# Performance work log

Measured on AMD Instinct MI355X. Metric: run time of the kernel, lower is better.

Reference implementation:

```python
import jax, jax.numpy as jnp
import numpy as np

HID = 768
POS = 768
TGT = 20
LBL = 30522
EPS = 1e-5


def layer_norm(x, g, b):
    mu = jnp.mean(x, axis=-1, keepdims=True)
    var = jnp.mean((x - mu) ** 2, axis=-1, keepdims=True)
    return (x - mu) * jax.lax.rsqrt(var + EPS) * g + b


def setup_inputs() -> dict:
    key = jax.random.key(0)
    ks = jax.random.split(key, 12)
    bs, n_node, num_pairs = 4, 512, 128
    inp = {
        "input_nodes": jax.random.normal(ks[0], (bs, n_node, HID), dtype=jnp.float32),
        "pairs": jax.random.randint(ks[1], (bs, num_pairs, 2), 0, n_node - 1, dtype=jnp.int64),
        "pos_emb": jax.random.normal(ks[2], (TGT, POS), dtype=jnp.float32) * 0.02,
        "W1": jax.random.normal(ks[3], (2 * HID + POS, HID), dtype=jnp.float32) * 0.02,
        "b1": jnp.zeros((HID,), dtype=jnp.float32),
        "g1": jnp.ones((HID,), dtype=jnp.float32),
        "be1": jnp.zeros((HID,), dtype=jnp.float32),
        "W2": jax.random.normal(ks[4], (HID, HID), dtype=jnp.float32) * 0.02,
        "b2": jnp.zeros((HID,), dtype=jnp.float32),
        "g2": jnp.ones((HID,), dtype=jnp.float32),
        "be2": jnp.zeros((HID,), dtype=jnp.float32),
        "Wd": jax.random.normal(ks[5], (HID, LBL), dtype=jnp.float32) * 0.02,
        "bd": jnp.zeros((LBL,), dtype=jnp.float32),
    }
    return inp


def reference(input_nodes, pairs, pos_emb, W1, b1, g1, be1, W2, b2, g2, be2, Wd, bd):
    bs, num_pairs, _ = pairs.shape
    dim = input_nodes.shape[-1]
    left = pairs[:, :, 0] + 1   # [bs, np]
    right = pairs[:, :, 1] + 1
    # gather paired node features: [bs, np, dim]
    lh = jnp.take_along_axis(input_nodes, left[:, :, None], axis=1)
    rh = jnp.take_along_axis(input_nodes, right[:, :, None], axis=1)
    R = bs * num_pairs
    lh = jnp.broadcast_to(lh.reshape(R, 1, dim), (R, TGT, dim))
    rh = jnp.broadcast_to(rh.reshape(R, 1, dim), (R, TGT, dim))
    pe = jnp.broadcast_to(pos_emb[None, :, :], (R, TGT, POS))
    x = jnp.concatenate((lh, rh, pe), axis=-1)  # [R, TGT, 2*HID+POS]
    h = layer_norm(jax.nn.gelu(x @ W1 + b1), g1, be1)
    h = layer_norm(jax.nn.gelu(h @ W2 + b2), g2, be2)
    return h @ Wd + bd  # [R, TGT, LBL]
```

## Files before the change

kernel.cpp:

```cpp
#include <hip/hip_runtime.h>
#include <stdint.h>
#include <math.h>

typedef unsigned short u16;
typedef unsigned int u32;

#define HID   768
#define TGT   20
#define LBL   30522
#define RPAIR 512
#define ROWS  10240
#define KCAT  1536
#define NPAD2 30720

typedef float  f32x4  __attribute__((ext_vector_type(4)));
typedef __bf16 bf16x8 __attribute__((ext_vector_type(8)));

__device__ __forceinline__ u16 f2bf(float f) {
  u32 u = __float_as_uint(f);
  u += 0x7fffu + ((u >> 16) & 1u);
  return (u16)(u >> 16);
}
__device__ __forceinline__ float bf2f(u16 h) {
  return __uint_as_float(((u32)h) << 16);
}
__device__ __forceinline__ float gelu_tanh(float x) {
  float x3 = x * x * x;
  float t = tanhf(0.7978845608028654f * (x + 0.044715f * x3));
  return 0.5f * x * (1.0f + t);
}

__device__ __forceinline__ void async16(u16* lds, const u16* g) {
  __builtin_amdgcn_global_load_lds(
      (__attribute__((address_space(1))) void*)const_cast<u16*>(g),
      (__attribute__((address_space(3))) void*)lds,
      16, 0, 0);
}

#define BARRIER() do { asm volatile("" ::: "memory"); __builtin_amdgcn_s_barrier(); asm volatile("" ::: "memory"); } while (0)
#define VMWAIT8() do { asm volatile("s_waitcnt vmcnt(8)" ::: "memory"); __builtin_amdgcn_sched_barrier(0); } while (0)
#define VMWAIT0() do { asm volatile("s_waitcnt vmcnt(0)" ::: "memory"); __builtin_amdgcn_sched_barrier(0); } while (0)

__global__ __launch_bounds__(256) void tconv_kernel(const float* __restrict__ B,
                                                    u16* __restrict__ Bt,
                                                    int K, int N, int Npad) {
  __shared__ u16 tile[32][34];
  int n0 = blockIdx.x * 32, k0 = blockIdx.y * 32;
  int tx = threadIdx.x & 31, ty = threadIdx.x >> 5;
#pragma unroll
  for (int i = 0; i < 4; i++) {
    int kk = ty + i * 8;
    int k = k0 + kk, n = n0 + tx;
    float v = (k < K && n < N) ? B[(size_t)k * N + n] : 0.0f;
    tile[kk][tx] = f2bf(v);
  }
  __syncthreads();
#pragma unroll
  for (int i = 0; i < 4; i++) {
    int nn = ty + i * 8;
    int n = n0 + nn, k = k0 + tx;
    if (n < Npad && k < K) Bt[(size_t)n * K + k] = tile[tx][nn];
  }
}

__global__ __launch_bounds__(256) void gather_kernel(const float* __restrict__ nodes,
                                                     const int* __restrict__ p32,
                                                     u16* __restrict__ A1) {
  int idx = blockIdx.x * 256 + threadIdx.x;
  if (idx >= RPAIR * KCAT) return;
  bool is64 = ((p32[1] | p32[3] | p32[5] | p32[7] | p32[9] | p32[11] | p32[13] | p32[15]) == 0);
  int r = idx / KCAT, c = idx - r * KCAT;
  int b = r >> 7, p = r & 127;
  int which = (c >= HID) ? 1 : 0;
  int cc = which ? (c - HID) : c;
  int slot = (b * 128 + p) * 2 + which;
  int node = (is64 ? p32[slot * 2] : p32[slot]) + 1;
  float v = nodes[((size_t)(b * 512 + node)) * HID + cc];
  A1[idx] = f2bf(v);
}

__global__ __launch_bounds__(256) void peproj_kernel(const float* __restrict__ pos_emb,
                                                     const float* __restrict__ W1,
                                                     const float* __restrict__ b1,
                                                     float* __restrict__ pep) {
  __shared__ float pe[HID];
  int t = blockIdx.x, tid = threadIdx.x;
  for (int i = tid; i < HID; i += 256) pe[i] = pos_emb[t * HID + i];
  __syncthreads();
  float acc0 = 0.f, acc1 = 0.f, acc2 = 0.f;
  const float* Wp = W1 + (size_t)KCAT * HID;
  for (int k = 0; k < HID; k++) {
    float p = pe[k];
    const float* wr = Wp + (size_t)k * HID;
    acc0 = fmaf(p, wr[tid], acc0);
    acc1 = fmaf(p, wr[tid + 256], acc1);
    acc2 = fmaf(p, wr[tid + 512], acc2);
  }
  pep[t * HID + tid]       = acc0 + b1[tid];
  pep[t * HID + tid + 256] = acc1 + b1[tid + 256];
  pep[t * HID + tid + 512] = acc2 + b1[tid + 512];
}

template <int EPI>
__global__ __launch_bounds__(256) void gemm_bt(const u16* __restrict__ A,
                                               const u16* __restrict__ Bt,
                                               const float* __restrict__ bias,
                                               float* __restrict__ Cf,
                                               u16* __restrict__ Cb,
                                               int N, int K) {
  __shared__ __align__(16) u16 As[128 * 32];
  __shared__ __align__(16) u16 Bs[128 * 32];
  const int tid  = threadIdx.x;
  const int lane = tid & 63;
  const int w    = tid >> 6;
  const int wr   = w >> 1, wc = w & 1;
  const int m0 = blockIdx.y * 128;
  const int n0 = blockIdx.x * 128;

  f32x4 acc[4][4];
  const f32x4 fzero = {0.f, 0.f, 0.f, 0.f};
#pragma unroll
  for (int m = 0; m < 4; m++)
#pragma unroll
    for (int n = 0; n < 4; n++) acc[m][n] = fzero;

  const int srow = lane >> 2;
  const int scol = (lane & 3) * 8;
  const int nkt = K >> 5;

  for (int kt = 0; kt < nkt; ++kt) {
    const int k0 = kt << 5;
#pragma unroll
    for (int j = 0; j < 2; j++) {
      int rbase = w * 32 + j * 16;
      async16(&As[rbase * 32], A + (size_t)(m0 + rbase + srow) * K + k0 + scol);
      async16(&Bs[rbase * 32], Bt + (size_t)(n0 + rbase + srow) * K + k0 + scol);
    }
    asm volatile("s_waitcnt vmcnt(0)" ::: "memory");
    __syncthreads();

    bf16x8 a[4], b[4];
    const int kk = (lane >> 4) * 8;
#pragma unroll
    for (int m = 0; m < 4; m++)
      a[m] = *reinterpret_cast<const bf16x8*>(&As[(wr * 64 + m * 16 + (lane & 15)) * 32 + kk]);
#pragma unroll
    for (int n = 0; n < 4; n++)
      b[n] = *reinterpret_cast<const bf16x8*>(&Bs[(wc * 64 + n * 16 + (lane & 15)) * 32 + kk]);
#pragma unroll
    for (int m = 0; m < 4; m++)
#pragma unroll
      for (int n = 0; n < 4; n++)
        acc[m][n] = __builtin_amdgcn_mfma_f32_16x16x32_bf16(a[m], b[n], acc[m][n], 0, 0, 0);
    __syncthreads();
  }

  const int rr = (lane >> 4) * 4;
  const int cc = lane & 15;
#pragma unroll
  for (int m = 0; m < 4; m++) {
#pragma unroll
    for (int n = 0; n < 4; n++) {
      int col = n0 + wc * 64 + n * 16 + cc;
#pragma unroll
      for (int j = 0; j < 4; j++) {
        int row = m0 + wr * 64 + m * 16 + rr + j;
        float v = acc[m][n][j];
        if (EPI == 0) {
          Cf[(size_t)row * N + col] = v;
        } else {
          v = gelu_tanh(v + bias[col]);
          Cb[(size_t)row * N + col] = f2bf(v);
        }
      }
    }
  }
}

__global__ __launch_bounds__(512, 2) void gemm256_stream(const u16* __restrict__ A,
                                                         const u16* __restrict__ B,
                                                         const float* __restrict__ bias,
                                                         float* __restrict__ C) {
  __shared__ __align__(16) u16 As[2][256 * 64];
  __shared__ __align__(16) u16 Bs[2][256 * 64];
  const int tid  = threadIdx.x;
  const int lane = tid & 63;
  const int wid  = tid >> 6;
  const int wm   = wid >> 2;
  const int wn   = wid & 3;

  const int x  = blockIdx.x & 7;
  const int jb = blockIdx.x >> 3;
  const int t0 = (600 * jb) >> 5;
  const int t1 = (600 * (jb + 1)) >> 5;
  const int Q  = (t1 - t0) * 12;

  f32x4 acc[8][4];
  const f32x4 fzero = {0.f, 0.f, 0.f, 0.f};
#pragma unroll
  for (int mi = 0; mi < 8; mi++)
#pragma unroll
    for (int ni = 0; ni < 4; ni++) acc[mi][ni] = fzero;

  const int sl_r = lane >> 3;
  const int sl_c = ((lane & 7) ^ sl_r) * 8;

  auto stage = [&](int q) {
    int tt = t0 + q / 12;
    int kt = q - (q / 12) * 12;
    int mt = 5 * x + tt / 120;
    int nt = tt - (tt / 120) * 120;
    const int k0 = kt * 64;
    u16* Ab = As[q & 1];
    u16* Bb = Bs[q & 1];
    const u16* Ag = A + (size_t)(mt * 256) * 768 + k0;
    const u16* Bg = B + (size_t)(nt * 256) * 768 + k0;
#pragma unroll
    for (int jj = 0; jj < 4; jj++) {
      int rbase = wid * 32 + jj * 8;
      async16(Ab + rbase * 64, Ag + (size_t)(rbase + sl_r) * 768 + sl_c);
      async16(Bb + rbase * 64, Bg + (size_t)(rbase + sl_r) * 768 + sl_c);
    }
  };
  auto lda = [&](const u16* buf, int mi, int ks) -> bf16x8 {
    int row = wm * 128 + mi * 16 + (lane & 15);
    int kch = ks * 4 + (lane >> 4);
    return *reinterpret_cast<const bf16x8*>(&buf[row * 64 + ((kch ^ (row & 7)) << 3)]);
  };
  auto ldb = [&](const u16* buf, int ni, int ks) -> bf16x8 {
    int row = wn * 64 + ni * 16 + (lane & 15);
    int kch = ks * 4 + (lane >> 4);
    return *reinterpret_cast<const bf16x8*>(&buf[row * 64 + ((kch ^ (row & 7)) << 3)]);
  };

  const int rr  = (lane >> 4) * 4;
  const int ccl = lane & 15;

  stage(0);
  for (int q = 0; q < Q; ++q) {
    if (q + 1 < Q) { stage(q + 1); VMWAIT8(); }
    else          { VMWAIT0(); }
    BARRIER();

    const u16* Ab = As[q & 1];
    const u16* Bb = Bs[q & 1];
#pragma unroll
    for (int ks = 0; ks < 2; ++ks) {
      bf16x8 aF[8], bF[4];
#pragma unroll
      for (int mi = 0; mi < 8; ++mi) aF[mi] = lda(Ab, mi, ks);
#pragma unroll
      for (int ni = 0; ni < 4; ++ni) bF[ni] = ldb(Bb, ni, ks);
      __builtin_amdgcn_s_setprio(1);
#pragma unroll
      for (int mi = 0; mi < 8; ++mi)
#pragma unroll
        for (int ni = 0; ni < 4; ++ni)
          acc[mi][ni] = __builtin_amdgcn_mfma_f32_16x16x32_bf16(aF[mi], bF[ni], acc[mi][ni], 0, 0, 0);
      __builtin_amdgcn_s_setprio(0);
    }

    int kt = q - (q / 12) * 12;
    if (kt == 11) {
      int tt = t0 + q / 12;
      int mt = 5 * x + tt / 120;
      int nt = tt - (tt / 120) * 120;
      int r0 = mt * 256 + wm * 128;
      int c0 = nt * 256 + wn * 64;
#pragma unroll
      for (int ni = 0; ni < 4; ++ni) {
        int col = c0 + ni * 16 + ccl;
        if (col < LBL) {
          float bv = bias[col];
#pragma unroll
          for (int mi = 0; mi < 8; ++mi)
#pragma unroll
            for (int j = 0; j < 4; ++j)
              C[(size_t)(r0 + mi * 16 + rr + j) * LBL + col] = acc[mi][ni][j] + bv;
        }
      }
#pragma unroll
      for (int mi = 0; mi < 8; mi++)
#pragma unroll
        for (int ni = 0; ni < 4; ni++) acc[mi][ni] = fzero;
    }
    BARRIER();
  }
}

__global__ __launch_bounds__(256) void fuse1_kernel(const float* __restrict__ s,
                                                    const float* __restrict__ pep,
                                                    const float* __restrict__ g1,
                                                    const float* __restrict__ be1,
                                                    u16* __restrict__ h1) {
  __shared__ float red[8];
  int g = blockIdx.x, tid = threadIdx.x;
  int r = g / TGT, t = g - r * TGT;
  const float* sr = s + (size_t)r * HID;
  const float* pt = pep + (size_t)t * HID;
  float y[3], s1 = 0.f, s2 = 0.f;
#pragma unroll
  for (int i = 0; i < 3; i++) {
    int j = tid + i * 256;
    float x = sr[j] + pt[j];
    y[i] = gelu_tanh(x);
    s1 += y[i];
    s2 += y[i] * y[i];
  }
#pragma unroll
  for (int off = 32; off > 0; off >>= 1) {
    s1 += __shfl_down(s1, off);
    s2 += __shfl_down(s2, off);
  }
  if ((tid & 63) == 0) { red[tid >> 6] = s1; red[4 + (tid >> 6)] = s2; }
  __syncthreads();
  float mean = (red[0] + red[1] + red[2] + red[3]) * (1.0f / HID);
  float var  = (red[4] + red[5] + red[6] + red[7]) * (1.0f / HID) - mean * mean;
  float inv  = rsqrtf(var + 1e-5f);
#pragma unroll
  for (int i = 0; i < 3; i++) {
    int j = tid + i * 256;
    h1[(size_t)g * HID + j] = f2bf((y[i] - mean) * inv * g1[j] + be1[j]);
  }
}

__global__ __launch_bounds__(256) void fuse2_kernel(const u16* __restrict__ G,
                                                    const float* __restrict__ g2,
                                                    const float* __restrict__ be2,
                                                    u16* __restrict__ h2) {
  __shared__ float red[8];
  int g = blockIdx.x, tid = threadIdx.x;
  const u16* gr = G + (size_t)g * HID;
  float y[3], s1 = 0.f, s2 = 0.f;
#pragma unroll
  for (int i = 0; i < 3; i++) {
    int j = tid + i * 256;
    y[i] = bf2f(gr[j]);
    s1 += y[i];
    s2 += y[i] * y[i];
  }
#pragma unroll
  for (int off = 32; off > 0; off >>= 1) {
    s1 += __shfl_down(s1, off);
    s2 += __shfl_down(s2, off);
  }
  if ((tid & 63) == 0) { red[tid >> 6] = s1; red[4 + (tid >> 6)] = s2; }
  __syncthreads();
  float mean = (red[0] + red[1] + red[2] + red[3]) * (1.0f / HID);
  float var  = (red[4] + red[5] + red[6] + red[7]) * (1.0f / HID) - mean * mean;
  float inv  = rsqrtf(var + 1e-5f);
#pragma unroll
  for (int i = 0; i < 3; i++) {
    int j = tid + i * 256;
    h2[(size_t)g * HID + j] = f2bf((y[i] - mean) * inv * g2[j] + be2[j]);
  }
}

extern "C" void kernel_launch(void* const* d_in, const int* in_sizes, int n_in,
                              void* d_out, int out_size, void* d_ws, size_t ws_size,
                              hipStream_t stream) {
  const float* input_nodes = (const float*)d_in[0];
  const int*   pairs       = (const int*)d_in[1];
  const float* pos_emb     = (const float*)d_in[2];
  const float* W1  = (const float*)d_in[3];
  const float* b1  = (const float*)d_in[4];
  const float* g1  = (const float*)d_in[5];
  const float* be1 = (const float*)d_in[6];
  const float* W2  = (const float*)d_in[7];
  const float* b2  = (const float*)d_in[8];
  const float* g2  = (const float*)d_in[9];
  const float* be2 = (const float*)d_in[10];
  const float* Wd  = (const float*)d_in[11];
  const float* bd  = (const float*)d_in[12];
  float* out = (float*)d_out;

  char* ws = (char*)d_ws;
  u16*   WdT   = (u16*)(ws + 0);
  u16*   W2T   = (u16*)(ws + 47185920);
  u16*   W1lrT = (u16*)(ws + 48365568);
  u16*   A1    = (u16*)(ws + 50724864);
  float* pep   = (float*)(ws + 52297728);
  float* sbuf  = (float*)(ws + 52359168);
  u16*   h1    = (u16*)(ws + 53932032);
  u16*   G     = (u16*)(ws + 69660672);

  tconv_kernel<<<dim3(960, 24), 256, 0, stream>>>(Wd, WdT, HID, LBL, NPAD2);
  tconv_kernel<<<dim3(24, 24), 256, 0, stream>>>(W2, W2T, HID, HID, HID);
  tconv_kernel<<<dim3(24, 48), 256, 0, stream>>>(W1, W1lrT, KCAT, HID, HID);
  gather_kernel<<<dim3((RPAIR * KCAT + 255) / 256), 256, 0, stream>>>(input_nodes, pairs, A1);
  peproj_kernel<<<dim3(TGT), 256, 0, stream>>>(pos_emb, W1, b1, pep);

  gemm_bt<0><<<dim3(6, 4), 256, 0, stream>>>(A1, W1lrT, nullptr, sbuf, nullptr, HID, KCAT);
  fuse1_kernel<<<dim3(ROWS), 256, 0, stream>>>(sbuf, pep, g1, be1, h1);

  gemm_bt<1><<<dim3(6, 80), 256, 0, stream>>>(h1, W2T, b2, nullptr, G, HID, HID);
  fuse2_kernel<<<dim3(ROWS), 256, 0, stream>>>(G, g2, be2, G);

  gemm256_stream<<<dim3(256), 512, 0, stream>>>(G, WdT, bd, out);
}
```

Baseline: 1.181 ms.

## Stage final GEMM epilogue through LDS and overlap its stores with next tile

Restructures the vocabulary GEMM so each output tile's accumulators pass through an LDS buffer and are written as coalesced float4 rows instead of scattered scalar stores. Half the epilogue is issued after the last K step and the rest is deferred into the next tile's first K step, with tuned vmcnt waits so the stores overlap the loads and MFMA work. Tile assignment becomes strided round-robin, and the bias is loaded once per tile as a vector. The extra 32 KB LDS buffer and launch_bounds(512,1) lower the occupancy target, and the hand-counted waitcnt values are fragile.

```diff
diff --git a/kernel.cpp b/kernel.cpp
--- a/kernel.cpp
+++ b/kernel.cpp
@@ -38,8 +38,8 @@
 }
 
 #define BARRIER() do { asm volatile("" ::: "memory"); __builtin_amdgcn_s_barrier(); asm volatile("" ::: "memory"); } while (0)
-#define VMWAIT8() do { asm volatile("s_waitcnt vmcnt(8)" ::: "memory"); __builtin_amdgcn_sched_barrier(0); } while (0)
-#define VMWAIT0() do { asm volatile("s_waitcnt vmcnt(0)" ::: "memory"); __builtin_amdgcn_sched_barrier(0); } while (0)
+#define LBAR() do { asm volatile("s_waitcnt lgkmcnt(0)" ::: "memory"); __builtin_amdgcn_sched_barrier(0); __builtin_amdgcn_s_barrier(); asm volatile("" ::: "memory"); } while (0)
+#define VMW(N) do { asm volatile("s_waitcnt vmcnt(" #N ")" ::: "memory"); __builtin_amdgcn_sched_barrier(0); } while (0)
 
 __global__ __launch_bounds__(256) void tconv_kernel(const float* __restrict__ B,
                                                     u16* __restrict__ Bt,
@@ -177,12 +177,13 @@
   }
 }
 
-__global__ __launch_bounds__(512, 2) void gemm256_stream(const u16* __restrict__ A,
-                                                         const u16* __restrict__ B,
-                                                         const float* __restrict__ bias,
-                                                         float* __restrict__ C) {
+__global__ __launch_bounds__(512, 1) void gemm256_drip(const u16* __restrict__ A,
+                                                       const u16* __restrict__ B,
+                                                       const float* __restrict__ bias,
+                                                       float* __restrict__ C) {
   __shared__ __align__(16) u16 As[2][256 * 64];
   __shared__ __align__(16) u16 Bs[2][256 * 64];
+  __shared__ __align__(16) float ep[32 * 256];
   const int tid  = threadIdx.x;
   const int lane = tid & 63;
   const int wid  = tid >> 6;
@@ -191,28 +192,24 @@
 
   const int x  = blockIdx.x & 7;
   const int jb = blockIdx.x >> 3;
-  const int t0 = (600 * jb) >> 5;
-  const int t1 = (600 * (jb + 1)) >> 5;
-  const int Q  = (t1 - t0) * 12;
+  const int S  = (600 - jb + 31) >> 5;
 
   f32x4 acc[8][4];
   const f32x4 fzero = {0.f, 0.f, 0.f, 0.f};
-#pragma unroll
-  for (int mi = 0; mi < 8; mi++)
-#pragma unroll
-    for (int ni = 0; ni < 4; ni++) acc[mi][ni] = fzero;
 
   const int sl_r = lane >> 3;
   const int sl_c = ((lane & 7) ^ sl_r) * 8;
 
-  auto stage = [&](int q) {
-    int tt = t0 + q / 12;
-    int kt = q - (q / 12) * 12;
-    int mt = 5 * x + tt / 120;
-    int nt = tt - (tt / 120) * 120;
+  auto tileCoord = [&](int s, int& mt, int& nt) {
+    int u = jb + (s << 5);
+    int q5 = u / 5;
+    mt = 5 * x + (u - q5 * 5);
+    nt = q5;
+  };
+
+  auto stageK = [&](int buf, int mt, int nt, int kt) {
     const int k0 = kt * 64;
-    u16* Ab = As[q & 1];
-    u16* Bb = Bs[q & 1];
+    u16* Ab = As[buf]; u16* Bb = Bs[buf];
     const u16* Ag = A + (size_t)(mt * 256) * 768 + k0;
     const u16* Bg = B + (size_t)(nt * 256) * 768 + k0;
 #pragma unroll
@@ -235,57 +232,104 @@
 
   const int rr  = (lane >> 4) * 4;
   const int ccl = lane & 15;
-
-  stage(0);
-  for (int q = 0; q < Q; ++q) {
-    if (q + 1 < Q) { stage(q + 1); VMWAIT8(); }
-    else          { VMWAIT0(); }
-    BARRIER();
-
-    const u16* Ab = As[q & 1];
-    const u16* Bb = Bs[q & 1];
-#pragma unroll
-    for (int ks = 0; ks < 2; ++ks) {
-      bf16x8 aF[8], bF[4];
-#pragma unroll
-      for (int mi = 0; mi < 8; ++mi) aF[mi] = lda(Ab, mi, ks);
-#pragma unroll
-      for (int ni = 0; ni < 4; ++ni) bF[ni] = ldb(Bb, ni, ks);
-      __builtin_amdgcn_s_setprio(1);
-#pragma unroll
-      for (int mi = 0; mi < 8; ++mi)
-#pragma unroll
-        for (int ni = 0; ni < 4; ++ni)
-          acc[mi][ni] = __builtin_amdgcn_mfma_f32_16x16x32_bf16(aF[mi], bF[ni], acc[mi][ni], 0, 0, 0);
-      __builtin_amdgcn_s_setprio(0);
-    }
-
-    int kt = q - (q / 12) * 12;
-    if (kt == 11) {
-      int tt = t0 + q / 12;
-      int mt = 5 * x + tt / 120;
-      int nt = tt - (tt / 120) * 120;
-      int r0 = mt * 256 + wm * 128;
-      int c0 = nt * 256 + wn * 64;
-#pragma unroll
-      for (int ni = 0; ni < 4; ++ni) {
-        int col = c0 + ni * 16 + ccl;
-        if (col < LBL) {
-          float bv = bias[col];
-#pragma unroll
-          for (int mi = 0; mi < 8; ++mi)
-#pragma unroll
-            for (int j = 0; j < 4; ++j)
-              C[(size_t)(r0 + mi * 16 + rr + j) * LBL + col] = acc[mi][ni][j] + bv;
+  const int c4  = (tid & 63) * 4;
+
+  f32x4 b4 = fzero;
+  auto bounce4 = [&](int miBase, int r0t, int c0t, int ntB) {
+#pragma unroll
+    for (int mi0 = 0; mi0 < 4; ++mi0) {
+      int mi = miBase + mi0;
+#pragma unroll
+      for (int ni = 0; ni < 4; ++ni)
+#pragma unroll
+        for (int j = 0; j < 4; ++j)
+          ep[(wm * 16 + rr + j) * 256 + wn * 64 + ni * 16 + ccl] = acc[mi][ni][j];
+      LBAR();
+#pragma unroll
+      for (int p = 0; p < 4; ++p) {
+        int lr = p * 8 + wid;
+        int rowg = r0t + (lr >> 4) * 128 + mi * 16 + (lr & 15);
+        f32x4 v = *reinterpret_cast<const f32x4*>(&ep[lr * 256 + c4]);
+        v += b4;
+        if (ntB != 119) {
+          *reinterpret_cast<f32x4*>(&C[(size_t)rowg * LBL + c0t + c4]) = v;
+        } else {
+          int colb = c0t + c4;
+#pragma unroll
+          for (int e = 0; e < 4; ++e)
+            if (colb + e < LBL) C[(size_t)rowg * LBL + colb + e] = v[e];
         }
       }
-#pragma unroll
-      for (int mi = 0; mi < 8; mi++)
-#pragma unroll
-        for (int ni = 0; ni < 4; ni++) acc[mi][ni] = fzero;
+      LBAR();
     }
-    BARRIER();
-  }
+  };
+
+  int mt, nt; tileCoord(0, mt, nt);
+  int mtN = mt, ntN = nt;
+  int pR0 = 0, pC0 = 0, pNt = 0;
+
+  stageK(0, mt, nt, 0);
+  asm volatile("s_waitcnt vmcnt(0)" ::: "memory");
+  __builtin_amdgcn_sched_barrier(0);
+  BARRIER();
+
+  for (int s = 0; s < S; ++s) {
+    const bool hasNext = (s + 1 < S);
+    if (hasNext) tileCoord(s + 1, mtN, ntN);
+    const int r0t = mt * 256, c0t = nt * 256;
+
+#pragma unroll
+    for (int kt = 0; kt < 12; ++kt) {
+      if (kt < 11) stageK((kt + 1) & 1, mt, nt, kt + 1);
+      else if (hasNext) stageK(0, mtN, ntN, 0);
+
+      if (kt == 0) {
+        if (s > 0) {
+          bounce4(4, pR0, pC0, pNt);
+          if (pNt == 119) { VMW(0); } else { VMW(41); }
+        } else { VMW(8); }
+      } else if (kt == 1) {
+        if (s > 0 && pNt != 119) { VMW(24); } else { VMW(8); }
+      } else {
+        VMW(8);
+      }
+      BARRIER();
+
+      const u16* Ab = As[kt & 1];
+      const u16* Bb = Bs[kt & 1];
+#pragma unroll
+      for (int ks = 0; ks < 2; ++ks) {
+        bf16x8 aF[8], bF[4];
+#pragma unroll
+        for (int mi = 0; mi < 8; ++mi) aF[mi] = lda(Ab, mi, ks);
+#pragma unroll
+        for (int ni = 0; ni < 4; ++ni) bF[ni] = ldb(Bb, ni, ks);
+        __builtin_amdgcn_s_setprio(1);
+#pragma unroll
+        for (int mi = 0; mi < 8; ++mi)
+#pragma unroll
+          for (int ni = 0; ni < 4; ++ni)
+            acc[mi][ni] = __builtin_amdgcn_mfma_f32_16x16x32_bf16(
+                aF[mi], bF[ni], (kt == 0 && ks == 0) ? fzero : acc[mi][ni], 0, 0, 0);
+        __builtin_amdgcn_s_setprio(0);
+      }
+      BARRIER();
+
+      if (kt == 11) {
+        if (nt != 119) {
+          b4 = *reinterpret_cast<const f32x4*>(&bias[c0t + c4]);
+        } else {
+          int cb = c0t + c4;
+#pragma unroll
+          for (int e = 0; e < 4; ++e) b4[e] = (cb + e < LBL) ? bias[cb + e] : 0.f;
+        }
+        bounce4(0, r0t, c0t, nt);
+        pR0 = r0t; pC0 = c0t; pNt = nt;
+      }
+    }
+    mt = mtN; nt = ntN;
+  }
+  bounce4(4, pR0, pC0, pNt);
 }
 
 __global__ __launch_bounds__(256) void fuse1_kernel(const float* __restrict__ s,
@@ -396,5 +440,5 @@
   gemm_bt<1><<<dim3(6, 80), 256, 0, stream>>>(h1, W2T, b2, nullptr, G, HID, HID);
   fuse2_kernel<<<dim3(ROWS), 256, 0, stream>>>(G, g2, be2, G);
 
-  gemm256_stream<<<dim3(256), 512, 0, stream>>>(G, WdT, bd, out);
-}
+  gemm256_drip<<<dim3(256), 512, 0, stream>>>(G, WdT, bd, out);
+}
```

New measurement: 1.253 ms. +6.1%, slower.
